# Optimization experiments

Hardware: AMD Instinct MI355X
Metric: run time of the kernel (lower is better)

## Reference

```python
import jax, jax.numpy as jnp
import numpy as np

NLAYERS = 2
K = 8          # number of attention heads
H = 64         # hidden_size (per-head QK dim)
D = 1024       # input_size; value head dim = D // K = 128
B = 4
L = 1024


def setup_inputs() -> dict:
    key = jax.random.key(0)
    ks = jax.random.split(key, 5)
    s = 1.0 / np.sqrt(D).astype(np.float32)
    return {
        "x": jax.random.normal(ks[0], (B, L, D), jnp.float32),
        "Wq": jax.random.normal(ks[1], (NLAYERS, D, H * K), jnp.float32) * s,
        "bq": jnp.zeros((NLAYERS, H * K), jnp.float32),
        "Wk": jax.random.normal(ks[2], (NLAYERS, D, H * K), jnp.float32) * s,
        "bk": jnp.zeros((NLAYERS, H * K), jnp.float32),
    }


def reference(x, Wq, bq, Wk, bk):
    Bb, Ll, Dd = x.shape
    scale = 1.0 / np.sqrt(H).astype(np.float32)
    # strictly lower-triangular causal mask: torch.tril(-1)
    causal = jnp.tril(jnp.ones((Ll, Ll), x.dtype), -1)
    neg = 1e30 * (1.0 - causal)  # additive mask
    out = x
    graphs, outputs = [], []
    for i in range(NLAYERS):
        q = jax.nn.relu(out @ Wq[i] + bq[i]).reshape(Bb, Ll, K, H)
        k = jax.nn.relu(out @ Wk[i] + bk[i]).reshape(Bb, Ll, K, H)
        att = jnp.einsum('bqkh,bskh->bkqs', q, k) * scale - neg  # [B,K,L,L]
        att = jax.nn.softmax(att, axis=-1)
        v = out.reshape(Bb, Ll, K, Dd // K)                      # value = hidden itself
        cur = jnp.einsum('bkqs,bskd->bqkd', att, v).reshape(Bb, Ll, Dd)
        out = out + cur  # residual (use_gru=False)
        graphs.append(att)
        outputs.append(out)
    return jnp.stack(graphs, 0), jnp.stack(outputs, 0)
```

## Files before the change

### kernel.cpp

```cpp
#include <hip/hip_runtime.h>
#include <cstdint>
#include <cstddef>

typedef float  f32x4  __attribute__((ext_vector_type(4)));
typedef short  bf16x8 __attribute__((ext_vector_type(8)));
typedef unsigned int u32;
typedef __attribute__((address_space(1))) const u32 gu32;
typedef __attribute__((address_space(3))) u32 su32;

constexpr int Bc = 4, Lc = 1024, Dc = 1024, Kc = 8, Hc = 64, NHc = 512;
constexpr float SCALE = 0.125f;
constexpr long long GSZ = 2LL * Bc * Kc * Lc * Lc;
constexpr long long OSZ = (long long)Bc * Lc * Dc;
constexpr int QB = 16;

__device__ __forceinline__ unsigned short f2bf(float f) {
    unsigned u = __float_as_uint(f);
    u += 0x7fffu + ((u >> 16) & 1u);
    return (unsigned short)(u >> 16);
}
__device__ __forceinline__ float bf2f(unsigned short s) {
    return __uint_as_float((unsigned)s << 16);
}

__device__ __forceinline__ void bar_lds() {
    asm volatile("s_waitcnt lgkmcnt(0)" ::: "memory");
    __builtin_amdgcn_s_barrier();
    __builtin_amdgcn_sched_barrier(0);
}

__global__ __launch_bounds__(256)
void cast_bf16(const float* __restrict__ in, unsigned short* __restrict__ outp, int n)
{
    const int i = (blockIdx.x * 256 + threadIdx.x) * 8;
    if (i >= n) return;
    float4 a = *(const float4*)(in + i);
    float4 b = *(const float4*)(in + i + 4);
    bf16x8 v;
    v[0] = (short)f2bf(a.x); v[1] = (short)f2bf(a.y);
    v[2] = (short)f2bf(a.z); v[3] = (short)f2bf(a.w);
    v[4] = (short)f2bf(b.x); v[5] = (short)f2bf(b.y);
    v[6] = (short)f2bf(b.z); v[7] = (short)f2bf(b.w);
    *(bf16x8*)(outp + i) = v;
}

__global__ __launch_bounds__(256)
void wtrans(const float* __restrict__ Wq, const float* __restrict__ Wk,
            float* __restrict__ outbase)
{
    __shared__ float Tl[64][68];
    const int z = blockIdx.z, layer = z >> 1, m = z & 1;
    const float* src = (m ? Wk : Wq) + (size_t)layer * Dc * NHc;
    unsigned short* dst = (unsigned short*)(outbase + (size_t)layer * (GSZ / 2))
                          + (size_t)m * NHc * Dc;
    const int k0 = blockIdx.x * 64, n0 = blockIdx.y * 64;
    const int t = threadIdx.x;
    {
        const int r0 = t >> 4, c0 = (t & 15) * 4;
        #pragma unroll
        for (int i = 0; i < 4; ++i)
            *(float4*)&Tl[r0 + 16 * i][c0] =
                *(const float4*)&src[(size_t)(k0 + r0 + 16 * i) * NHc + n0 + c0];
    }
    __syncthreads();
    {
        const int nn = t >> 2, ks = (t & 3) * 16;
        bf16x8 v0, v1;
        #pragma unroll
        for (int j = 0; j < 8; ++j) v0[j] = (short)f2bf(Tl[ks + j][nn]);
        #pragma unroll
        for (int j = 0; j < 8; ++j) v1[j] = (short)f2bf(Tl[ks + 8 + j][nn]);
        unsigned short* dp = dst + (size_t)(n0 + nn) * Dc + k0 + ks;
        *(bf16x8*)dp       = v0;
        *(bf16x8*)(dp + 8) = v1;
    }
}

__global__ __launch_bounds__(512)
void qk_gemm(const unsigned short* __restrict__ hidb,
             const unsigned short* __restrict__ Wtq, const unsigned short* __restrict__ Wtk,
             const float* __restrict__ bq, const float* __restrict__ bk,
             unsigned short* __restrict__ qbuf, unsigned short* __restrict__ kbuf)
{
    __shared__ unsigned short As[2][128][32];
    __shared__ unsigned short Bs[2][128][32];

    const unsigned short* Wt = blockIdx.z ? Wtk : Wtq;
    const float* bi = blockIdx.z ? bk : bq;
    unsigned short* C = blockIdx.z ? kbuf : qbuf;
    const int m0 = blockIdx.x * 128, n0 = blockIdx.y * 128;
    const int t = threadIdx.x, lane = t & 63, w = t >> 6;
    const int lr = lane & 15, lg = lane >> 4;
    const int wmloc = (w >> 2) * 64, wnloc = (w & 3) * 32;

    const int arow = w * 16 + (lane >> 2);
    const int aslot = (lane & 3) ^ ((lane >> 3) & 3);
    const unsigned short* Ag = hidb + (size_t)(m0 + arow) * Dc + aslot * 8;
    const unsigned short* Bg = Wt   + (size_t)(n0 + arow) * Dc + aslot * 8;

    f32x4 acc[4][2] = {};
    const int slr = lg ^ ((lr >> 1) & 3);

    __builtin_amdgcn_global_load_lds((const gu32*)Ag, (su32*)&As[0][w * 16][0], 16, 0, 0);
    __builtin_amdgcn_global_load_lds((const gu32*)Bg, (su32*)&Bs[0][w * 16][0], 16, 0, 0);

    for (int it = 0; it < 32; ++it) {
        const int buf = it & 1;
        __syncthreads();
        if (it < 31) {
            const int koff = (it + 1) * 32;
            __builtin_amdgcn_global_load_lds((const gu32*)(Ag + koff),
                                             (su32*)&As[buf ^ 1][w * 16][0], 16, 0, 0);
            __builtin_amdgcn_global_load_lds((const gu32*)(Bg + koff),
                                             (su32*)&Bs[buf ^ 1][w * 16][0], 16, 0, 0);
        }
        bf16x8 a[4], bfr[2];
        #pragma unroll
        for (int mi = 0; mi < 4; ++mi)
            a[mi] = *(const bf16x8*)&As[buf][wmloc + mi * 16 + lr][slr * 8];
        #pragma unroll
        for (int ni = 0; ni < 2; ++ni)
            bfr[ni] = *(const bf16x8*)&Bs[buf][wnloc + ni * 16 + lr][slr * 8];
        #pragma unroll
        for (int mi = 0; mi < 4; ++mi)
            #pragma unroll
            for (int ni = 0; ni < 2; ++ni)
                acc[mi][ni] = __builtin_amdgcn_mfma_f32_16x16x32_bf16(a[mi], bfr[ni], acc[mi][ni], 0, 0, 0);
    }

    #pragma unroll
    for (int ni = 0; ni < 2; ++ni) {
        const int gc = n0 + wnloc + ni * 16 + lr;
        const float bv = bi[gc];
        #pragma unroll
        for (int mi = 0; mi < 4; ++mi)
            #pragma unroll
            for (int r = 0; r < 4; ++r) {
                const int row = m0 + wmloc + mi * 16 + lg * 4 + r;
                float v = fmaxf(acc[mi][ni][r] + bv, 0.0f);
                C[(size_t)row * NHc + gc] = f2bf(v);
            }
    }
}

__global__ __launch_bounds__(512, 6)
void attn_fused(const unsigned short* __restrict__ qbuf,
                const unsigned short* __restrict__ kbuf,
                const unsigned short* __restrict__ hidb,
                const float* __restrict__ res,
                float* __restrict__ att, float* __restrict__ outp,
                unsigned short* __restrict__ hidnext)
{
    __shared__ unsigned short Sb[QB][1032];
    union KVU {
        unsigned short KS[128][72];
        unsigned short VS[64][136];
    };
    __shared__ KVU kv;

    const int id = blockIdx.x;
    const int kh = id & 7, slot = (id >> 3) & 63, b = id >> 9;
    const int qt = (slot == 0) ? 0 : 64 - slot;
    const int q0 = qt * QB;
    const int t = threadIdx.x, lane = t & 63, w = t >> 6;
    const int lr = lane & 15, lg = lane >> 4;

    bf16x8 aq[2];
    #pragma unroll
    for (int ks = 0; ks < 2; ++ks)
        aq[ks] = *(const bf16x8*)(qbuf + (size_t)(b * Lc + q0 + lr) * NHc + kh * Hc + ks * 32 + lg * 8);

    const int ccount = (q0 + QB + 63) >> 6;
    const int nchunk2 = (ccount + 1) >> 1;

    const int krow = t >> 2, kcol = (t & 3) * 16;
    for (int c2 = 0; c2 < nchunk2; ++c2) {
        const unsigned short* kp = kbuf + (size_t)(b * Lc + c2 * 128 + krow) * NHc + kh * Hc + kcol;
        *(bf16x8*)&kv.KS[krow][kcol]     = *(const bf16x8*)kp;
        *(bf16x8*)&kv.KS[krow][kcol + 8] = *(const bf16x8*)(kp + 8);
        bar_lds();
        f32x4 acc = {};
        __builtin_amdgcn_s_setprio(1);
        #pragma unroll
        for (int ks = 0; ks < 2; ++ks) {
            bf16x8 bfr = *(const bf16x8*)&kv.KS[w * 16 + lr][ks * 32 + lg * 8];
            acc = __builtin_amdgcn_mfma_f32_16x16x32_bf16(aq[ks], bfr, acc, 0, 0, 0);
        }
        __builtin_amdgcn_s_setprio(0);
        #pragma unroll
        for (int r = 0; r < 4; ++r)
            Sb[lg * 4 + r][c2 * 128 + w * 16 + lr] = f2bf(acc[r] * SCALE);
        bar_lds();
    }

    #pragma unroll
    for (int i = 0; i < 2; ++i) {
        const int row = w * 2 + i, qrow = q0 + row;
        float* orow = att + ((size_t)(b * Kc + kh) * Lc + qrow) * Lc;
        if (qrow == 0) {
            const float u = 1.0f / 1024.0f;
            const short ub = (short)f2bf(u);
            bf16x8 pv8;
            #pragma unroll
            for (int j = 0; j < 8; ++j) pv8[j] = ub;
            #pragma unroll
            for (int tt = 0; tt < 2; ++tt) {
                const int col = lane * 8 + tt * 512;
                float4 o = { u, u, u, u };
                *(float4*)(orow + col) = o;
                *(float4*)(orow + col + 4) = o;
                *(bf16x8*)&Sb[row][col] = pv8;
            }
            continue;
        }
        float mx = -3.0e38f;
        #pragma unroll
        for (int tt = 0; tt < 2; ++tt) {
            const int col = lane * 8 + tt * 512;
            bf16x8 v = *(const bf16x8*)&Sb[row][col];
            #pragma unroll
            for (int j = 0; j < 8; ++j)
                if (col + j < qrow) mx = fmaxf(mx, bf2f((unsigned short)v[j]));
        }
        #pragma unroll
        for (int off = 1; off < 64; off <<= 1) mx = fmaxf(mx, __shfl_xor(mx, off));
        float sum = 0.0f;
        #pragma unroll
        for (int tt = 0; tt < 2; ++tt) {
            const int col = lane * 8 + tt * 512;
            bf16x8 v = *(const bf16x8*)&Sb[row][col];
            #pragma unroll
            for (int j = 0; j < 8; ++j)
                sum += (col + j < qrow) ? __expf(bf2f((unsigned short)v[j]) - mx) : 0.0f;
        }
        #pragma unroll
        for (int off = 1; off < 64; off <<= 1) sum += __shfl_xor(sum, off);
        const float inv = 1.0f / sum;
        #pragma unroll
        for (int tt = 0; tt < 2; ++tt) {
            const int col = lane * 8 + tt * 512;
            bf16x8 v = *(const bf16x8*)&Sb[row][col];
            float e[8];
            #pragma unroll
            for (int j = 0; j < 8; ++j)
                e[j] = (col + j < qrow) ? __expf(bf2f((unsigned short)v[j]) - mx) * inv : 0.0f;
            float4 o0 = { e[0], e[1], e[2], e[3] };
            float4 o1 = { e[4], e[5], e[6], e[7] };
            *(float4*)(orow + col) = o0;
            *(float4*)(orow + col + 4) = o1;
            bf16x8 pb;
            #pragma unroll
            for (int j = 0; j < 8; ++j) pb[j] = (short)f2bf(e[j]);
            *(bf16x8*)&Sb[row][col] = pb;
        }
    }
    bar_lds();

    const int stiles = (qt == 0) ? 16 : ccount;
    f32x4 acc3 = {};
    const int dloc = w * 16 + lr, dcol = kh * 128 + dloc;
    const int vrow = t >> 3, vcol = (t & 7) * 8;
    const unsigned short* vb = hidb + (size_t)(b * Lc + vrow) * Dc + kh * 128 + vcol;
    for (int ti = 0; ti < stiles; ++ti) {
        const unsigned short* vp = vb + (size_t)ti * 64 * Dc;
        *(bf16x8*)&kv.VS[vrow][vcol]      = *(const bf16x8*)vp;
        *(bf16x8*)&kv.VS[vrow][vcol + 64] = *(const bf16x8*)(vp + 64);
        bar_lds();
        __builtin_amdgcn_s_setprio(1);
        #pragma unroll
        for (int ks = 0; ks < 2; ++ks) {
            bf16x8 pa = *(const bf16x8*)&Sb[lr][ti * 64 + ks * 32 + lg * 8];
            bf16x8 bb;
            #pragma unroll
            for (int j = 0; j < 8; ++j)
                bb[j] = (short)kv.VS[ks * 32 + lg * 8 + j][dloc];
            acc3 = __builtin_amdgcn_mfma_f32_16x16x32_bf16(pa, bb, acc3, 0, 0, 0);
        }
        __builtin_amdgcn_s_setprio(0);
        bar_lds();
    }

    #pragma unroll
    for (int r = 0; r < 4; ++r) {
        const size_t idx = (size_t)(b * Lc + q0 + lg * 4 + r) * Dc + dcol;
        const float v = res[idx] + acc3[r];
        outp[idx] = v;
        if (hidnext) hidnext[idx] = f2bf(v);
    }
}

extern "C" void kernel_launch(void* const* d_in, const int* in_sizes, int n_in,
                              void* d_out, int out_size, void* d_ws, size_t ws_size,
                              hipStream_t stream)
{
    const float* x  = (const float*)d_in[0];
    const float* Wq = (const float*)d_in[1];
    const float* bq = (const float*)d_in[2];
    const float* Wk = (const float*)d_in[3];
    const float* bk = (const float*)d_in[4];
    float* out = (float*)d_out;

    unsigned short* hidbA = (unsigned short*)d_ws;
    unsigned short* hidbB = hidbA + (size_t)Bc * Lc * Dc;
    unsigned short* qb    = hidbB + (size_t)Bc * Lc * Dc;
    unsigned short* kb    = qb    + (size_t)Bc * Lc * NHc;

    const int nhid = Bc * Lc * Dc;

    cast_bf16<<<nhid / 8 / 256, 256, 0, stream>>>(x, hidbA, nhid);
    wtrans<<<dim3(16, 8, 4), 256, 0, stream>>>(Wq, Wk, out);

    for (int l = 0; l < 2; ++l) {
        float* attL = out + (size_t)l * (GSZ / 2);
        float* outL = out + GSZ + (size_t)l * OSZ;
        const float* resL = l ? (out + GSZ) : x;
        const unsigned short* hidL = l ? hidbB : hidbA;
        const unsigned short* WtL = (const unsigned short*)attL;

        qk_gemm<<<dim3(32, 4, 2), 512, 0, stream>>>(
            hidL, WtL, WtL + (size_t)NHc * Dc, bq + l * NHc, bk + l * NHc, qb, kb);

        attn_fused<<<Bc * 64 * Kc, 512, 0, stream>>>(
            qb, kb, hidL, resL, attL, outL, l == 0 ? hidbB : (unsigned short*)nullptr);
    }
}
```

Before: 186.8 us.

## Double attention query tile to 32 rows to reuse K/V tiles across more queries

Raises the per-block query tile from 16 to 32 rows, halving the grid and reworking the QK and PV MFMA loops so each loaded K chunk and V tile serves two 16-row fragments. K chunks shrink to 64 rows and V tiles to 32 rows, and each warp now handles four softmax rows. The aim is to cut redundant global K/V reads and per-block overhead. The cost is a larger LDS footprint, lower occupancy (launch bound 6 to 4), fewer blocks for load balance, and finer-grained loops with more barriers.

After: 200.1 us. +7.1%, slower.

```diff
diff --git a/kernel.cpp b/kernel.cpp
--- a/kernel.cpp
+++ b/kernel.cpp
@@ -12,7 +12,7 @@
 constexpr float SCALE = 0.125f;
 constexpr long long GSZ = 2LL * Bc * Kc * Lc * Lc;
 constexpr long long OSZ = (long long)Bc * Lc * Dc;
-constexpr int QB = 16;
+constexpr int QB = 32;
 
 __device__ __forceinline__ unsigned short f2bf(float f) {
     unsigned u = __float_as_uint(f);
@@ -143,7 +143,7 @@
     }
 }
 
-__global__ __launch_bounds__(512, 6)
+__global__ __launch_bounds__(512, 4)
 void attn_fused(const unsigned short* __restrict__ qbuf,
                 const unsigned short* __restrict__ kbuf,
                 const unsigned short* __restrict__ hidb,
@@ -153,49 +153,51 @@
 {
     __shared__ unsigned short Sb[QB][1032];
     union KVU {
-        unsigned short KS[128][72];
-        unsigned short VS[64][136];
+        unsigned short KS[64][72];
+        unsigned short VS[32][136];
     };
     __shared__ KVU kv;
 
     const int id = blockIdx.x;
-    const int kh = id & 7, slot = (id >> 3) & 63, b = id >> 9;
-    const int qt = (slot == 0) ? 0 : 64 - slot;
+    const int kh = id & 7, slot = (id >> 3) & 31, b = id >> 8;
+    const int qt = (slot == 0) ? 0 : 32 - slot;
     const int q0 = qt * QB;
     const int t = threadIdx.x, lane = t & 63, w = t >> 6;
     const int lr = lane & 15, lg = lane >> 4;
 
-    bf16x8 aq[2];
+    bf16x8 aq[2][2];
     #pragma unroll
-    for (int ks = 0; ks < 2; ++ks)
-        aq[ks] = *(const bf16x8*)(qbuf + (size_t)(b * Lc + q0 + lr) * NHc + kh * Hc + ks * 32 + lg * 8);
+    for (int mf = 0; mf < 2; ++mf)
+        #pragma unroll
+        for (int ks = 0; ks < 2; ++ks)
+            aq[mf][ks] = *(const bf16x8*)(qbuf + (size_t)(b * Lc + q0 + mf * 16 + lr) * NHc
+                                          + kh * Hc + ks * 32 + lg * 8);
 
     const int ccount = (q0 + QB + 63) >> 6;
-    const int nchunk2 = (ccount + 1) >> 1;
-
-    const int krow = t >> 2, kcol = (t & 3) * 16;
-    for (int c2 = 0; c2 < nchunk2; ++c2) {
-        const unsigned short* kp = kbuf + (size_t)(b * Lc + c2 * 128 + krow) * NHc + kh * Hc + kcol;
-        *(bf16x8*)&kv.KS[krow][kcol]     = *(const bf16x8*)kp;
-        *(bf16x8*)&kv.KS[krow][kcol + 8] = *(const bf16x8*)(kp + 8);
+
+    const int krow = t >> 3, kcol = (t & 7) * 8;
+    const int mfw = w >> 2, niw = w & 3;
+    for (int c = 0; c < ccount; ++c) {
+        const unsigned short* kp = kbuf + (size_t)(b * Lc + c * 64 + krow) * NHc + kh * Hc + kcol;
+        *(bf16x8*)&kv.KS[krow][kcol] = *(const bf16x8*)kp;
         bar_lds();
         f32x4 acc = {};
         __builtin_amdgcn_s_setprio(1);
         #pragma unroll
         for (int ks = 0; ks < 2; ++ks) {
-            bf16x8 bfr = *(const bf16x8*)&kv.KS[w * 16 + lr][ks * 32 + lg * 8];
-            acc = __builtin_amdgcn_mfma_f32_16x16x32_bf16(aq[ks], bfr, acc, 0, 0, 0);
+            bf16x8 bfr = *(const bf16x8*)&kv.KS[niw * 16 + lr][ks * 32 + lg * 8];
+            acc = __builtin_amdgcn_mfma_f32_16x16x32_bf16(aq[mfw][ks], bfr, acc, 0, 0, 0);
         }
         __builtin_amdgcn_s_setprio(0);
         #pragma unroll
         for (int r = 0; r < 4; ++r)
-            Sb[lg * 4 + r][c2 * 128 + w * 16 + lr] = f2bf(acc[r] * SCALE);
+            Sb[mfw * 16 + lg * 4 + r][c * 64 + niw * 16 + lr] = f2bf(acc[r] * SCALE);
         bar_lds();
     }
 
     #pragma unroll
-    for (int i = 0; i < 2; ++i) {
-        const int row = w * 2 + i, qrow = q0 + row;
+    for (int i = 0; i < 4; ++i) {
+        const int row = w * 4 + i, qrow = q0 + row;
         float* orow = att + ((size_t)(b * Kc + kh) * Lc + qrow) * Lc;
         if (qrow == 0) {
             const float u = 1.0f / 1024.0f;
@@ -256,37 +258,37 @@
     }
     bar_lds();
 
-    const int stiles = (qt == 0) ? 16 : ccount;
-    f32x4 acc3 = {};
+    const int ntiles = (qt == 0) ? 32 : ((q0 + 62) >> 5);
+    f32x4 acc3[2] = {};
     const int dloc = w * 16 + lr, dcol = kh * 128 + dloc;
-    const int vrow = t >> 3, vcol = (t & 7) * 8;
+    const int vrow = t >> 4, vcol = (t & 15) * 8;
     const unsigned short* vb = hidb + (size_t)(b * Lc + vrow) * Dc + kh * 128 + vcol;
-    for (int ti = 0; ti < stiles; ++ti) {
-        const unsigned short* vp = vb + (size_t)ti * 64 * Dc;
-        *(bf16x8*)&kv.VS[vrow][vcol]      = *(const bf16x8*)vp;
-        *(bf16x8*)&kv.VS[vrow][vcol + 64] = *(const bf16x8*)(vp + 64);
+    for (int ti = 0; ti < ntiles; ++ti) {
+        *(bf16x8*)&kv.VS[vrow][vcol] = *(const bf16x8*)(vb + (size_t)ti * 32 * Dc);
         bar_lds();
         __builtin_amdgcn_s_setprio(1);
-        #pragma unroll
-        for (int ks = 0; ks < 2; ++ks) {
-            bf16x8 pa = *(const bf16x8*)&Sb[lr][ti * 64 + ks * 32 + lg * 8];
-            bf16x8 bb;
-            #pragma unroll
-            for (int j = 0; j < 8; ++j)
-                bb[j] = (short)kv.VS[ks * 32 + lg * 8 + j][dloc];
-            acc3 = __builtin_amdgcn_mfma_f32_16x16x32_bf16(pa, bb, acc3, 0, 0, 0);
+        bf16x8 bb;
+        #pragma unroll
+        for (int j = 0; j < 8; ++j)
+            bb[j] = (short)kv.VS[lg * 8 + j][dloc];
+        #pragma unroll
+        for (int mf = 0; mf < 2; ++mf) {
+            bf16x8 pa = *(const bf16x8*)&Sb[mf * 16 + lr][ti * 32 + lg * 8];
+            acc3[mf] = __builtin_amdgcn_mfma_f32_16x16x32_bf16(pa, bb, acc3[mf], 0, 0, 0);
         }
         __builtin_amdgcn_s_setprio(0);
         bar_lds();
     }
 
     #pragma unroll
-    for (int r = 0; r < 4; ++r) {
-        const size_t idx = (size_t)(b * Lc + q0 + lg * 4 + r) * Dc + dcol;
-        const float v = res[idx] + acc3[r];
-        outp[idx] = v;
-        if (hidnext) hidnext[idx] = f2bf(v);
-    }
+    for (int mf = 0; mf < 2; ++mf)
+        #pragma unroll
+        for (int r = 0; r < 4; ++r) {
+            const size_t idx = (size_t)(b * Lc + q0 + mf * 16 + lg * 4 + r) * Dc + dcol;
+            const float v = res[idx] + acc3[mf][r];
+            outp[idx] = v;
+            if (hidnext) hidnext[idx] = f2bf(v);
+        }
 }
 
 extern "C" void kernel_launch(void* const* d_in, const int* in_sizes, int n_in,
@@ -320,7 +322,7 @@
         qk_gemm<<<dim3(32, 4, 2), 512, 0, stream>>>(
             hidL, WtL, WtL + (size_t)NHc * Dc, bq + l * NHc, bk + l * NHc, qb, kb);
 
-        attn_fused<<<Bc * 64 * Kc, 512, 0, stream>>>(
+        attn_fused<<<Bc * 32 * Kc, 512, 0, stream>>>(
             qb, kb, hidL, resL, attL, outL, l == 0 ? hidbB : (unsigned short*)nullptr);
     }
 }
```

## Transpose hidden state to bf16 column-major for vectorized V loads in attention

Applied to the files above, without the earlier changes.

Adds a per-layer kernel that casts the residual hidden state to bf16 and transposes it to [B, D, L]. The attention PV loop then loads V tiles as contiguous rows into a transposed LDS buffer and reads each MFMA B-operand with one vector load instead of eight strided scalar LDS reads. This trades extra global traffic for the transpose pass against cheaper LDS access in the PV loop. The LDS row stride of 66 elements may misalign the 16-byte vector reads.

Measured after the change: 279.8 us. 49.7% more time.

```diff
diff --git a/kernel.cpp b/kernel.cpp
--- a/kernel.cpp
+++ b/kernel.cpp
@@ -45,6 +45,33 @@
 }
 
 __global__ __launch_bounds__(256)
+void cast_tr(const float* __restrict__ src, unsigned short* __restrict__ hidT)
+{
+    __shared__ float Tl[64][68];
+    const int b = blockIdx.z, s0 = blockIdx.x * 64, d0 = blockIdx.y * 64;
+    const int t = threadIdx.x;
+    {
+        const int r = t >> 4, c = (t & 15) * 4;
+        #pragma unroll
+        for (int i = 0; i < 4; ++i)
+            *(float4*)&Tl[r + 16 * i][c] =
+                *(const float4*)&src[((size_t)(b * Lc + s0 + r + 16 * i)) * Dc + d0 + c];
+    }
+    __syncthreads();
+    {
+        const int d = t >> 2, sc = (t & 3) * 16;
+        bf16x8 v0, v1;
+        #pragma unroll
+        for (int j = 0; j < 8; ++j) v0[j] = (short)f2bf(Tl[sc + j][d]);
+        #pragma unroll
+        for (int j = 0; j < 8; ++j) v1[j] = (short)f2bf(Tl[sc + 8 + j][d]);
+        unsigned short* dp = hidT + ((size_t)(b * Dc + d0 + d)) * Lc + s0 + sc;
+        *(bf16x8*)dp       = v0;
+        *(bf16x8*)(dp + 8) = v1;
+    }
+}
+
+__global__ __launch_bounds__(256)
 void wtrans(const float* __restrict__ Wq, const float* __restrict__ Wk,
             float* __restrict__ outbase)
 {
@@ -146,7 +173,7 @@
 __global__ __launch_bounds__(512, 6)
 void attn_fused(const unsigned short* __restrict__ qbuf,
                 const unsigned short* __restrict__ kbuf,
-                const unsigned short* __restrict__ hidb,
+                const unsigned short* __restrict__ hidT,
                 const float* __restrict__ res,
                 float* __restrict__ att, float* __restrict__ outp,
                 unsigned short* __restrict__ hidnext)
@@ -154,7 +181,7 @@
     __shared__ unsigned short Sb[QB][1032];
     union KVU {
         unsigned short KS[128][72];
-        unsigned short VS[64][136];
+        unsigned short VT[128][66];
     };
     __shared__ KVU kv;
 
@@ -259,21 +286,18 @@
     const int stiles = (qt == 0) ? 16 : ccount;
     f32x4 acc3 = {};
     const int dloc = w * 16 + lr, dcol = kh * 128 + dloc;
-    const int vrow = t >> 3, vcol = (t & 7) * 8;
-    const unsigned short* vb = hidb + (size_t)(b * Lc + vrow) * Dc + kh * 128 + vcol;
+    const int vd = t >> 2, vsc = (t & 3) * 16;
+    const unsigned short* vbase = hidT + (size_t)(b * Dc + kh * 128 + vd) * Lc + vsc;
     for (int ti = 0; ti < stiles; ++ti) {
-        const unsigned short* vp = vb + (size_t)ti * 64 * Dc;
-        *(bf16x8*)&kv.VS[vrow][vcol]      = *(const bf16x8*)vp;
-        *(bf16x8*)&kv.VS[vrow][vcol + 64] = *(const bf16x8*)(vp + 64);
+        const unsigned short* vp = vbase + ti * 64;
+        *(bf16x8*)&kv.VT[vd][vsc]     = *(const bf16x8*)vp;
+        *(bf16x8*)&kv.VT[vd][vsc + 8] = *(const bf16x8*)(vp + 8);
         bar_lds();
         __builtin_amdgcn_s_setprio(1);
         #pragma unroll
         for (int ks = 0; ks < 2; ++ks) {
             bf16x8 pa = *(const bf16x8*)&Sb[lr][ti * 64 + ks * 32 + lg * 8];
-            bf16x8 bb;
-            #pragma unroll
-            for (int j = 0; j < 8; ++j)
-                bb[j] = (short)kv.VS[ks * 32 + lg * 8 + j][dloc];
+            bf16x8 bb = *(const bf16x8*)&kv.VT[dloc][ks * 32 + lg * 8];
             acc3 = __builtin_amdgcn_mfma_f32_16x16x32_bf16(pa, bb, acc3, 0, 0, 0);
         }
         __builtin_amdgcn_s_setprio(0);
@@ -314,13 +338,16 @@
         float* attL = out + (size_t)l * (GSZ / 2);
         float* outL = out + GSZ + (size_t)l * OSZ;
         const float* resL = l ? (out + GSZ) : x;
+        const float* srcL = l ? (out + GSZ) : x;
         const unsigned short* hidL = l ? hidbB : hidbA;
         const unsigned short* WtL = (const unsigned short*)attL;
 
         qk_gemm<<<dim3(32, 4, 2), 512, 0, stream>>>(
             hidL, WtL, WtL + (size_t)NHc * Dc, bq + l * NHc, bk + l * NHc, qb, kb);
 
+        cast_tr<<<dim3(16, 16, 4), 256, 0, stream>>>(srcL, hidbA);
+
         attn_fused<<<Bc * 64 * Kc, 512, 0, stream>>>(
-            qb, kb, hidL, resL, attL, outL, l == 0 ? hidbB : (unsigned short*)nullptr);
-    }
-}
+            qb, kb, hidbA, resL, attL, outL, l == 0 ? hidbB : (unsigned short*)nullptr);
+    }
+}
```

## Double-buffer V tiles via async global_load_lds with XOR-swizzled LDS layout

Applied to the files above, without the earlier changes.

The PV loop now loads V tiles with direct global-to-LDS async loads into a double buffer. The next tile is prefetched while the current one is multiplied, and the first tile is issued before the softmax phase so its load overlaps that work. The LDS layout drops padding and uses an XOR swizzle to avoid bank conflicts. One barrier per iteration is removed. Launch bounds occupancy drops from 6 to 4 blocks per CU to make room for the larger LDS footprint and extra registers.

Result: slower. 195.9 us (+4.9%).

```diff
diff --git a/kernel.cpp b/kernel.cpp
--- a/kernel.cpp
+++ b/kernel.cpp
@@ -25,6 +25,11 @@
 
 __device__ __forceinline__ void bar_lds() {
     asm volatile("s_waitcnt lgkmcnt(0)" ::: "memory");
+    __builtin_amdgcn_s_barrier();
+    __builtin_amdgcn_sched_barrier(0);
+}
+__device__ __forceinline__ void bar_vm() {
+    asm volatile("s_waitcnt vmcnt(0) lgkmcnt(0)" ::: "memory");
     __builtin_amdgcn_s_barrier();
     __builtin_amdgcn_sched_barrier(0);
 }
@@ -143,7 +148,7 @@
     }
 }
 
-__global__ __launch_bounds__(512, 6)
+__global__ __launch_bounds__(512, 4)
 void attn_fused(const unsigned short* __restrict__ qbuf,
                 const unsigned short* __restrict__ kbuf,
                 const unsigned short* __restrict__ hidb,
@@ -154,7 +159,7 @@
     __shared__ unsigned short Sb[QB][1032];
     union KVU {
         unsigned short KS[128][72];
-        unsigned short VS[64][136];
+        unsigned short VS[2][64][128];
     };
     __shared__ KVU kv;
 
@@ -193,6 +198,13 @@
         bar_lds();
     }
 
+    const int vsrow = w * 8 + (lane >> 4);
+    const int vslot = (lane & 15) ^ w;
+    const unsigned short* vsrc0 = hidb + (size_t)(b * Lc + vsrow) * Dc + kh * 128 + vslot * 8;
+    const unsigned short* vsrc1 = vsrc0 + (size_t)4 * Dc;
+    __builtin_amdgcn_global_load_lds((const gu32*)vsrc0, (su32*)&kv.VS[0][w * 8][0], 16, 0, 0);
+    __builtin_amdgcn_global_load_lds((const gu32*)vsrc1, (su32*)&kv.VS[0][w * 8 + 4][0], 16, 0, 0);
+
     #pragma unroll
     for (int i = 0; i < 2; ++i) {
         const int row = w * 2 + i, qrow = q0 + row;
@@ -259,25 +271,30 @@
     const int stiles = (qt == 0) ? 16 : ccount;
     f32x4 acc3 = {};
     const int dloc = w * 16 + lr, dcol = kh * 128 + dloc;
-    const int vrow = t >> 3, vcol = (t & 7) * 8;
-    const unsigned short* vb = hidb + (size_t)(b * Lc + vrow) * Dc + kh * 128 + vcol;
+    const int rdbase = w * 2 + (lr >> 3);
+    const int col0 = ((rdbase ^ lg) << 3) + (lr & 7);
     for (int ti = 0; ti < stiles; ++ti) {
-        const unsigned short* vp = vb + (size_t)ti * 64 * Dc;
-        *(bf16x8*)&kv.VS[vrow][vcol]      = *(const bf16x8*)vp;
-        *(bf16x8*)&kv.VS[vrow][vcol + 64] = *(const bf16x8*)(vp + 64);
-        bar_lds();
+        const int buf = ti & 1;
+        bar_vm();
+        if (ti + 1 < stiles) {
+            const size_t off = (size_t)(ti + 1) * 64 * Dc;
+            __builtin_amdgcn_global_load_lds((const gu32*)(vsrc0 + off),
+                                             (su32*)&kv.VS[buf ^ 1][w * 8][0], 16, 0, 0);
+            __builtin_amdgcn_global_load_lds((const gu32*)(vsrc1 + off),
+                                             (su32*)&kv.VS[buf ^ 1][w * 8 + 4][0], 16, 0, 0);
+        }
         __builtin_amdgcn_s_setprio(1);
         #pragma unroll
         for (int ks = 0; ks < 2; ++ks) {
             bf16x8 pa = *(const bf16x8*)&Sb[lr][ti * 64 + ks * 32 + lg * 8];
+            const int cc = col0 ^ (ks * 32);
             bf16x8 bb;
             #pragma unroll
             for (int j = 0; j < 8; ++j)
-                bb[j] = (short)kv.VS[ks * 32 + lg * 8 + j][dloc];
+                bb[j] = (short)kv.VS[buf][ks * 32 + lg * 8 + j][cc];
             acc3 = __builtin_amdgcn_mfma_f32_16x16x32_bf16(pa, bb, acc3, 0, 0, 0);
         }
         __builtin_amdgcn_s_setprio(0);
-        bar_lds();
     }
 
     #pragma unroll
```
